# Kernel optimization log

Hardware: AMD Instinct MI355X
Metric: run time of the kernel (lower is better)

The kernel has to match this reference:

```python
import jax, jax.numpy as jnp
import numpy as np

N_NODES = 100000
N_EDGES = 100000
NNZ = 3200000
D_IN, D_HID, N_CLS = 512, 16, 7
NEG_SLOPE = 0.2


def _segment_softmax(scores, seg, num_segments, sorted_seg):
    m = jax.ops.segment_max(scores, seg, num_segments=num_segments,
                            indices_are_sorted=sorted_seg)
    ex = jnp.exp(scores - m[seg])
    s = jax.ops.segment_sum(ex, seg, num_segments=num_segments,
                            indices_are_sorted=sorted_seg)
    return ex / (s[seg] + 1e-9)


def _hypergat_layer(X, W, a1, a2, node_idx, edge_idx):
    # X: [N, din] -> h: [N, dout]
    h = X @ W
    hv = h[node_idx]                                   # [nnz, dout] gather
    # phase 1: node -> hyperedge attention (softmax within each hyperedge)
    s1 = jax.nn.leaky_relu(hv @ a1, NEG_SLOPE)         # [nnz]
    alpha = _segment_softmax(s1, edge_idx, N_EDGES, True)
    e = jax.ops.segment_sum(alpha[:, None] * hv, edge_idx,
                            num_segments=N_EDGES, indices_are_sorted=True)
    # phase 2: hyperedge -> node attention (softmax over edges incident to node)
    ev = e[edge_idx]                                   # [nnz, dout] gather
    s2 = jax.nn.leaky_relu(jnp.concatenate([hv, ev], axis=-1) @ a2, NEG_SLOPE)
    beta = _segment_softmax(s2, node_idx, N_NODES, False)
    out = jax.ops.segment_sum(beta[:, None] * ev, node_idx,
                              num_segments=N_NODES)
    return out


def setup_inputs() -> dict:
    key = jax.random.key(0)
    ks = jax.random.split(key, 8)
    H = jax.random.normal(ks[0], (N_NODES, D_IN), dtype=jnp.float32)
    node_idx = jax.random.randint(ks[1], (NNZ,), 0, N_NODES)
    edge_idx = jnp.sort(jax.random.randint(ks[2], (NNZ,), 0, N_EDGES))
    g1 = 1.0 / np.sqrt(D_IN)
    g2 = 1.0 / np.sqrt(D_HID)
    W1 = jax.random.uniform(ks[3], (D_IN, D_HID), jnp.float32, -g1, g1)
    a1_1 = jax.random.uniform(ks[4], (D_HID,), jnp.float32, -g2, g2)
    a2_1 = jax.random.uniform(ks[5], (2 * D_HID,), jnp.float32, -g2, g2)
    W2 = jax.random.uniform(ks[6], (D_HID, N_CLS), jnp.float32, -g2, g2)
    k7, k8 = jax.random.split(ks[7])
    gc = 1.0 / np.sqrt(N_CLS)
    a1_2 = jax.random.uniform(k7, (N_CLS,), jnp.float32, -gc, gc)
    a2_2 = jax.random.uniform(k8, (2 * N_CLS,), jnp.float32, -gc, gc)
    return {"H": H, "W1": W1, "a1_1": a1_1, "a2_1": a2_1,
            "W2": W2, "a1_2": a1_2, "a2_2": a2_2,
            "node_idx": node_idx, "edge_idx": edge_idx}


def reference(H, W1, a1_1, a2_1, W2, a1_2, a2_2, node_idx, edge_idx):
    H1 = _hypergat_layer(H, W1, a1_1, a2_1, node_idx, edge_idx)   # [N, 16]
    X2 = jax.nn.elu(H1)                                           # dropout off (eval)
    H2 = _hypergat_layer(X2, W2, a1_2, a2_2, node_idx, edge_idx)  # [N, 7]
    logp = jax.nn.log_softmax(H2, axis=1)
    return (logp, H1, H2)
```

## Files before the change

kernel.cpp:

```cpp
#include <hip/hip_runtime.h>
#include <hip/hip_bf16.h>
#include <math.h>

#define N_NODES 100000
#define N_EDGESC 100000
#define NNZ_C   3200000
#define D_IN    512
#define D_HID   16
#define N_CLS   7
#define NBK     782

#define G_GEMM 1563
#define G_HIST 1000
#define G_EOFF 3125
#define G_BIN  1000

typedef short short8 __attribute__((ext_vector_type(8)));
typedef float f32x4  __attribute__((ext_vector_type(4)));

__device__ __forceinline__ unsigned short f2bf_rn(float x) {
  unsigned int u = __float_as_uint(x);
  u += 0x7fff + ((u >> 16) & 1);
  return (unsigned short)(u >> 16);
}
__device__ __forceinline__ float bf2f(unsigned short b) {
  return __uint_as_float(((unsigned int)b) << 16);
}

__device__ __forceinline__ void eoff_body(int b, const int* __restrict__ eidx,
                                          int* __restrict__ eoff) {
  int i0 = (b * 256 + threadIdx.x) * 4;
  if (i0 >= NNZ_C) return;
  int4 v4 = *(const int4*)(eidx + i0);
  int vv[4] = {v4.x, v4.y, v4.z, v4.w};
  int prev = (i0 == 0) ? -1 : eidx[i0 - 1];
#pragma unroll
  for (int k = 0; k < 4; ++k) {
    for (int e = prev + 1; e <= vv[k]; ++e) eoff[e] = i0 + k;
    prev = vv[k];
  }
  if (i0 + 4 == NNZ_C) {
    for (int e = prev + 1; e <= N_EDGESC; ++e) eoff[e] = NNZ_C;
  }
}

__device__ __forceinline__ void hist_body(int b, const int* __restrict__ nidx,
                                          int* __restrict__ gcnt) {
  __shared__ int lh[NBK];
  int t = threadIdx.x;
  for (int i = t; i < NBK; i += 256) lh[i] = 0;
  __syncthreads();
  int base = b * 3200, end = base + 3200;
  for (int i = base + t; i < end; i += 256) atomicAdd(&lh[nidx[i] >> 7], 1);
  __syncthreads();
  for (int i = t; i < NBK; i += 256) {
    int c = lh[i];
    if (c) atomicAdd(&gcnt[i], c);
  }
}

__device__ __forceinline__ void bin_body(int b, const int* __restrict__ nidx,
                                         const int* __restrict__ eidx,
                                         int* __restrict__ bcur, int* __restrict__ binned) {
  __shared__ int lh[NBK];
  __shared__ int gb[NBK];
  int t = threadIdx.x;
  for (int i = t; i < NBK; i += 256) lh[i] = 0;
  __syncthreads();
  int base = b * 3200, end = base + 3200;
  for (int i = base + t; i < end; i += 256) atomicAdd(&lh[nidx[i] >> 7], 1);
  __syncthreads();
  for (int i = t; i < NBK; i += 256) {
    int c = lh[i];
    gb[i] = c ? atomicAdd(&bcur[i], c) : 0;
    lh[i] = 0;
  }
  __syncthreads();
  for (int i = base + t; i < end; i += 256) {
    int v = nidx[i], e = eidx[i];
    int bk = v >> 7;
    int r = atomicAdd(&lh[bk], 1);
    binned[gb[bk] + r] = e | ((v & 127) << 20);
  }
}

__global__ void bscan_kernel(const int* __restrict__ gcnt, int* __restrict__ boff,
                             int* __restrict__ bcur) {
  __shared__ int lds[1024];
  int t = threadIdx.x;
  int v = (t < NBK) ? gcnt[t] : 0;
  lds[t] = v;
  __syncthreads();
  for (int d = 1; d < 1024; d <<= 1) {
    int u = (t >= d) ? lds[t - d] : 0;
    __syncthreads();
    lds[t] += u;
    __syncthreads();
  }
  if (t < NBK) {
    boff[t + 1] = lds[t];
    bcur[t] = lds[t] - v;
  }
  if (t == 0) boff[0] = 0;
}

__global__ void csr_kernel(const int* __restrict__ binned, const int* __restrict__ boff,
                           int* __restrict__ noff, int* __restrict__ perm_e, int N) {
  __shared__ int lh[128];
  __shared__ int lsc[128];
  __shared__ int lcur[128];
  int b = blockIdx.x;
  int t = threadIdx.x;
  int s = boff[b], e = boff[b + 1];
  if (t < 128) lh[t] = 0;
  __syncthreads();
  for (int i = s + t; i < e; i += 256) {
    atomicAdd(&lh[binned[i] >> 20], 1);
  }
  __syncthreads();
  if (t < 128) lsc[t] = lh[t];
  __syncthreads();
  for (int d = 1; d < 128; d <<= 1) {
    int u = (t < 128 && t >= d) ? lsc[t - d] : 0;
    __syncthreads();
    if (t < 128) lsc[t] += u;
    __syncthreads();
  }
  if (t < 128) {
    int excl = lsc[t] - lh[t];
    lcur[t] = excl;
    int n = b * 128 + t;
    if (n <= N) noff[n] = s + excl;
  }
  __syncthreads();
  for (int i = s + t; i < e; i += 256) {
    int p = binned[i];
    int r = atomicAdd(&lcur[p >> 20], 1);
    perm_e[s + r] = p & 0xFFFFF;
  }
}

__device__ __forceinline__ void gemm1_body(int b,
    const float* __restrict__ X, const float* __restrict__ W,
    const float* __restrict__ a1, const float* __restrict__ a2,
    float* __restrict__ Hout, float2* __restrict__ phv) {
  int wid = b * 4 + (threadIdx.x >> 6);
  if (wid >= 6250) return;
  int lane = threadIdx.x & 63;
  int col  = lane & 15;
  int quad = lane >> 4;

  short8 wh[16], wl[16];
#pragma unroll
  for (int c = 0; c < 16; ++c) {
#pragma unroll
    for (int j = 0; j < 8; ++j) {
      float w = W[(c * 32 + quad * 8 + j) * 16 + col];
      unsigned short h = f2bf_rn(w);
      wh[c][j] = (short)h;
      wl[c][j] = (short)f2bf_rn(w - bf2f(h));
    }
  }

  int rowbase = wid * 16;
  const float4* Xr = (const float4*)(X + (size_t)(rowbase + col) * D_IN) + quad * 2;

  f32x4 acc_hh = {0.f, 0.f, 0.f, 0.f};
  f32x4 acc_hl = {0.f, 0.f, 0.f, 0.f};
  f32x4 acc_lh = {0.f, 0.f, 0.f, 0.f};

  float4 A0 = Xr[0], A1 = Xr[1];
  float4 B0 = Xr[8], B1 = Xr[9];
#pragma unroll
  for (int c = 0; c < 16; ++c) {
    float4 C0 = B0, C1 = B1;
    if (c < 14) { C0 = Xr[(c + 2) * 8]; C1 = Xr[(c + 2) * 8 + 1]; }
    float xs[8] = {A0.x, A0.y, A0.z, A0.w, A1.x, A1.y, A1.z, A1.w};
    short8 ah, al;
#pragma unroll
    for (int j = 0; j < 8; ++j) {
      unsigned short h = f2bf_rn(xs[j]);
      ah[j] = (short)h;
      al[j] = (short)f2bf_rn(xs[j] - bf2f(h));
    }
    acc_hh = __builtin_amdgcn_mfma_f32_16x16x32_bf16(ah, wh[c], acc_hh, 0, 0, 0);
    acc_hl = __builtin_amdgcn_mfma_f32_16x16x32_bf16(ah, wl[c], acc_hl, 0, 0, 0);
    acc_lh = __builtin_amdgcn_mfma_f32_16x16x32_bf16(al, wh[c], acc_lh, 0, 0, 0);
    A0 = B0; A1 = B1; B0 = C0; B1 = C1;
  }

  float a1c = a1[col], a2c = a2[col];
#pragma unroll
  for (int r = 0; r < 4; ++r) {
    float v = acc_hh[r] + acc_hl[r] + acc_lh[r];
    int row = rowbase + quad * 4 + r;
    Hout[(size_t)row * 16 + col] = v;
    float p1 = v * a1c, p2 = v * a2c;
#pragma unroll
    for (int d = 1; d < 16; d <<= 1) { p1 += __shfl_xor(p1, d); p2 += __shfl_xor(p2, d); }
    if (col == 0) phv[row] = make_float2(p1, p2);
  }
}

__global__ __launch_bounds__(256) void k1_kernel(
    const float* __restrict__ X, const float* __restrict__ W1,
    const float* __restrict__ a1_1, const float* __restrict__ a2_1,
    float* __restrict__ Hout, float2* __restrict__ phv,
    const int* __restrict__ eidx, int* __restrict__ eoff,
    const int* __restrict__ nidx, int* __restrict__ gcnt) {
  int b = blockIdx.x;
  if (b < G_GEMM) {
    gemm1_body(b, X, W1, a1_1, a2_1, Hout, phv);
  } else if (b < G_GEMM + G_HIST) {
    hist_body(b - G_GEMM, nidx, gcnt);
  } else {
    eoff_body(b - G_GEMM - G_HIST, eidx, eoff);
  }
}

template <int D, int GROUP>
__device__ __forceinline__ void edge_body(
    const float* __restrict__ h, const float2* __restrict__ phv,
    const float* __restrict__ a2, const int* __restrict__ eoff,
    const int* __restrict__ nidx, float* __restrict__ eout,
    float* __restrict__ pe, int E, int wave, int lane) {
  constexpr int NG = 64 / GROUP;
  if (wave >= E) return;
  int o0 = eoff[wave], o1 = eoff[wave + 1];
  int g = lane / GROUP, t = lane % GROUP;
  if (o0 == o1) {
    if (g == 0) {
      if (t < D) eout[(size_t)wave * D + t] = 0.f;
      if (t == 0) pe[wave] = 0.f;
    }
    return;
  }
  float m = -1e30f, l = 0.f, acc = 0.f;
  for (int base = o0; base < o1; base += 64) {
    int nrem = o1 - base; if (nrem > 64) nrem = 64;
    int li = base + lane;
    int idx_l = nidx[li < o1 ? li : o1 - 1];
    for (int jb = 0; jb < nrem; jb += 2 * NG) {
      int j = jb + g;
      bool oka = j < nrem;
      bool okb = j + NG < nrem;
      int va = __shfl(idx_l, j);
      int vb = __shfl(idx_l, j + NG);
      float pa_ = phv[va].x;
      float pb_ = phv[vb].x;
      float ha = (t < D) ? h[(size_t)va * D + t] : 0.f;
      float hb = (t < D) ? h[(size_t)vb * D + t] : 0.f;
      float sa = oka ? (pa_ > 0.f ? pa_ : 0.2f * pa_) : -1e30f;
      float sb = okb ? (pb_ > 0.f ? pb_ : 0.2f * pb_) : -1e30f;
      float mn = fmaxf(m, fmaxf(sa, sb));
      float eo = __expf(m - mn);
      float exa = oka ? __expf(sa - mn) : 0.f;
      float exb = okb ? __expf(sb - mn) : 0.f;
      l = l * eo + exa + exb;
      acc = acc * eo + exa * ha + exb * hb;
      m = mn;
    }
  }
#pragma unroll
  for (int d = GROUP; d < 64; d <<= 1) {
    float mo = __shfl_xor(m, d), lo = __shfl_xor(l, d), ao = __shfl_xor(acc, d);
    float mn = fmaxf(m, mo);
    float e0 = __expf(m - mn), e1x = __expf(mo - mn);
    l = l * e0 + lo * e1x;
    acc = acc * e0 + ao * e1x;
    m = mn;
  }
  float val = acc / (l + 1e-9f);
  float pav = (t < D) ? val * a2[D + t] : 0.f;
#pragma unroll
  for (int d = 1; d < GROUP; d <<= 1) pav += __shfl_xor(pav, d);
  if (g == 0) {
    if (t < D) eout[(size_t)wave * D + t] = val;
    if (t == 0) pe[wave] = pav;
  }
}

template <int D, int GROUP>
__global__ __launch_bounds__(256) void edge_kernel(
    const float* __restrict__ h, const float2* __restrict__ phv,
    const float* __restrict__ a2, const int* __restrict__ eoff,
    const int* __restrict__ nidx, float* __restrict__ eout,
    float* __restrict__ pe, int E) {
  int wave = (blockIdx.x * blockDim.x + threadIdx.x) >> 6;
  edge_body<D, GROUP>(h, phv, a2, eoff, nidx, eout, pe, E, wave, threadIdx.x & 63);
}

__global__ __launch_bounds__(256) void k3_kernel(
    const int* __restrict__ nidx, const int* __restrict__ eidx,
    int* __restrict__ bcur, int* __restrict__ binned,
    const float* __restrict__ h1g, const float2* __restrict__ phv,
    const float* __restrict__ a2_1, const int* __restrict__ eoff,
    float* __restrict__ e1, float* __restrict__ pe) {
  int b = blockIdx.x;
  if (b < G_BIN) {
    bin_body(b, nidx, eidx, bcur, binned);
  } else {
    int wave = (b - G_BIN) * 4 + (threadIdx.x >> 6);
    edge_body<D_HID, 16>(h1g, phv, a2_1, eoff, nidx, e1, pe, N_EDGESC,
                         wave, threadIdx.x & 63);
  }
}

__global__ __launch_bounds__(256) void node1_kernel(
    float2* phv, const float* __restrict__ e1,
    const float* __restrict__ pe, const int* __restrict__ noff,
    const int* __restrict__ perm_e, float* __restrict__ H1out,
    float* __restrict__ h2g, const float* __restrict__ W2,
    const float* __restrict__ a1_2, const float* __restrict__ a2_2) {
  int wave = (blockIdx.x * blockDim.x + threadIdx.x) >> 6;
  int lane = threadIdx.x & 63;
  if (wave >= N_NODES) return;
  int o0 = noff[wave], o1 = noff[wave + 1];
  int g = lane >> 4, t = lane & 15;
  float ph = phv[wave].y;
  float m = -1e30f, l = 0.f, acc = 0.f;
  for (int base = o0; base < o1; base += 64) {
    int nrem = o1 - base; if (nrem > 64) nrem = 64;
    int li = base + lane;
    int idx_l = perm_e[li < o1 ? li : o1 - 1];
    for (int jb = 0; jb < nrem; jb += 8) {
      int j = jb + g;
      bool oka = j < nrem;
      bool okb = j + 4 < nrem;
      int ea = __shfl(idx_l, j);
      int eb = __shfl(idx_l, j + 4);
      float pa_ = ph + pe[ea];
      float pb_ = ph + pe[eb];
      float va = e1[(size_t)ea * 16 + t];
      float vb = e1[(size_t)eb * 16 + t];
      float sa = oka ? (pa_ > 0.f ? pa_ : 0.2f * pa_) : -1e30f;
      float sb = okb ? (pb_ > 0.f ? pb_ : 0.2f * pb_) : -1e30f;
      float mn = fmaxf(m, fmaxf(sa, sb));
      float eo = __expf(m - mn);
      float exa = oka ? __expf(sa - mn) : 0.f;
      float exb = okb ? __expf(sb - mn) : 0.f;
      l = l * eo + exa + exb;
      acc = acc * eo + exa * va + exb * vb;
      m = mn;
    }
  }
#pragma unroll
  for (int d = 16; d < 64; d <<= 1) {
    float mo = __shfl_xor(m, d), lo = __shfl_xor(l, d), ao = __shfl_xor(acc, d);
    float mn = fmaxf(m, mo);
    float ea = __expf(m - mn), eb = __expf(mo - mn);
    l = l * ea + lo * eb;
    acc = acc * ea + ao * eb;
    m = mn;
  }
  float val = acc / (l + 1e-9f);
  if (g == 0) H1out[(size_t)wave * 16 + t] = val;
  float x = val > 0.f ? val : expm1f(val);
  float p1 = 0.f, p2 = 0.f, myh2 = 0.f;
#pragma unroll
  for (int j = 0; j < N_CLS; ++j) {
    float term = x * W2[t * N_CLS + j];
#pragma unroll
    for (int d = 1; d < 16; d <<= 1) term += __shfl_xor(term, d);
    p1 += term * a1_2[j];
    p2 += term * a2_2[j];
    if (t == j) myh2 = term;
  }
  if (g == 0) {
    if (t < N_CLS) h2g[(size_t)wave * N_CLS + t] = myh2;
    if (t == 0) phv[wave] = make_float2(p1, p2);
  }
}

__global__ __launch_bounds__(256) void node2_kernel(
    const float2* __restrict__ phv, const float* __restrict__ e2,
    const float* __restrict__ pe, const int* __restrict__ noff,
    const int* __restrict__ perm_e, float* __restrict__ H2out,
    float* __restrict__ logp) {
  int wave = (blockIdx.x * blockDim.x + threadIdx.x) >> 6;
  int lane = threadIdx.x & 63;
  if (wave >= N_NODES) return;
  int o0 = noff[wave], o1 = noff[wave + 1];
  int g = lane >> 3, t = lane & 7;
  float ph = phv[wave].y;
  float m = -1e30f, l = 0.f, acc = 0.f;
  for (int base = o0; base < o1; base += 64) {
    int nrem = o1 - base; if (nrem > 64) nrem = 64;
    int li = base + lane;
    int idx_l = perm_e[li < o1 ? li : o1 - 1];
    for (int jb = 0; jb < nrem; jb += 16) {
      int j = jb + g;
      bool oka = j < nrem;
      bool okb = j + 8 < nrem;
      int ea = __shfl(idx_l, j);
      int eb = __shfl(idx_l, j + 8);
      float pa_ = ph + pe[ea];
      float pb_ = ph + pe[eb];
      float va = (t < N_CLS) ? e2[(size_t)ea * N_CLS + t] : 0.f;
      float vb = (t < N_CLS) ? e2[(size_t)eb * N_CLS + t] : 0.f;
      float sa = oka ? (pa_ > 0.f ? pa_ : 0.2f * pa_) : -1e30f;
      float sb = okb ? (pb_ > 0.f ? pb_ : 0.2f * pb_) : -1e30f;
      float mn = fmaxf(m, fmaxf(sa, sb));
      float eo = __expf(m - mn);
      float exa = oka ? __expf(sa - mn) : 0.f;
      float exb = okb ? __expf(sb - mn) : 0.f;
      l = l * eo + exa + exb;
      acc = acc * eo + exa * va + exb * vb;
      m = mn;
    }
  }
#pragma unroll
  for (int d = 8; d < 64; d <<= 1) {
    float mo = __shfl_xor(m, d), lo = __shfl_xor(l, d), ao = __shfl_xor(acc, d);
    float mn = fmaxf(m, mo);
    float ea = __expf(m - mn), eb = __expf(mo - mn);
    l = l * ea + lo * eb;
    acc = acc * ea + ao * eb;
    m = mn;
  }
  float val = acc / (l + 1e-9f);
  if (g == 0 && t < N_CLS) H2out[(size_t)wave * N_CLS + t] = val;
  float xm = (t < N_CLS) ? val : -1e30f;
#pragma unroll
  for (int d = 1; d < 8; d <<= 1) xm = fmaxf(xm, __shfl_xor(xm, d));
  float se = (t < N_CLS) ? __expf(val - xm) : 0.f;
#pragma unroll
  for (int d = 1; d < 8; d <<= 1) se += __shfl_xor(se, d);
  float lg = logf(se);
  if (g == 0 && t < N_CLS) logp[(size_t)wave * N_CLS + t] = val - xm - lg;
}

extern "C" void kernel_launch(void* const* d_in, const int* in_sizes, int n_in,
                              void* d_out, int out_size, void* d_ws, size_t ws_size,
                              hipStream_t stream) {
  const float* H    = (const float*)d_in[0];
  const float* W1   = (const float*)d_in[1];
  const float* a1_1 = (const float*)d_in[2];
  const float* a2_1 = (const float*)d_in[3];
  const float* W2   = (const float*)d_in[4];
  const float* a1_2 = (const float*)d_in[5];
  const float* a2_2 = (const float*)d_in[6];
  const int* nidx   = (const int*)d_in[7];
  const int* eidx   = (const int*)d_in[8];

  float* outp = (float*)d_out;
  float* logp = outp;
  float* H1   = outp + (size_t)N_NODES * N_CLS;
  float* H2   = H1 + (size_t)N_NODES * D_HID;

  char* ws = (char*)d_ws;
  float* h1g  = (float*)(ws + 0);
  float* e1   = (float*)(ws + 6400000);
  float* h2g  = (float*)(ws + 12800000);
  float* e2   = (float*)(ws + 15600000);
  int* eoff   = (int*)(ws + 18400000);
  int* noff   = (int*)(ws + 18800128);
  float* pe   = (float*)(ws + 19200256);
  int* perm_e = (int*)(ws + 19600384);
  float2* phv = (float2*)(ws + 32400384);
  int* gcnt   = (int*)(ws + 33200384);
  int* boff   = (int*)(ws + 33203584);
  int* bcur   = (int*)(ws + 33206784);
  int* binned = (int*)(ws + 33210368);

  const int TB = 256;

  hipMemsetAsync(gcnt, 0, NBK * sizeof(int), stream);
  k1_kernel<<<G_GEMM + G_HIST + G_EOFF, TB, 0, stream>>>(
      H, W1, a1_1, a2_1, h1g, phv, eidx, eoff, nidx, gcnt);
  bscan_kernel<<<1, 1024, 0, stream>>>(gcnt, boff, bcur);
  k3_kernel<<<G_BIN + 25000, TB, 0, stream>>>(
      nidx, eidx, bcur, binned, h1g, phv, a2_1, eoff, e1, pe);
  csr_kernel<<<NBK, TB, 0, stream>>>(binned, boff, noff, perm_e, N_NODES);
  node1_kernel<<<25000, TB, 0, stream>>>(phv, e1, pe, noff, perm_e, H1, h2g,
                                         W2, a1_2, a2_2);
  edge_kernel<N_CLS, 8><<<25000, TB, 0, stream>>>(h2g, phv, a2_2, eoff, nidx, e2, pe, N_EDGESC);
  node2_kernel<<<25000, TB, 0, stream>>>(phv, e2, pe, noff, perm_e, H2, logp);
}
```

Before: 627.1 us.

## Pack layer-2 score scalars into padded 8-wide rows and unroll gather loops

Layer-2 node features and edge features are stored as 8-float rows with the attention projection scalar in the eighth slot, so one gather returns both value and score and a separate phv or pe lookup is avoided. Edge and node aggregation loops now process four neighbors per group per iteration instead of two, exposing more independent loads. The GEMM X prefetch is deepened from two chunks ahead to four. The costs are higher register pressure and padded buffers that use a little more memory traffic per row.

Result: no change. 622.5 us (-0.7%).

```diff
diff --git a/kernel.cpp b/kernel.cpp
--- a/kernel.cpp
+++ b/kernel.cpp
@@ -169,13 +169,14 @@
   f32x4 acc_hl = {0.f, 0.f, 0.f, 0.f};
   f32x4 acc_lh = {0.f, 0.f, 0.f, 0.f};
 
-  float4 A0 = Xr[0], A1 = Xr[1];
-  float4 B0 = Xr[8], B1 = Xr[9];
+  float4 pre[4][2];
+#pragma unroll
+  for (int q = 0; q < 4; ++q) { pre[q][0] = Xr[q * 8]; pre[q][1] = Xr[q * 8 + 1]; }
 #pragma unroll
   for (int c = 0; c < 16; ++c) {
-    float4 C0 = B0, C1 = B1;
-    if (c < 14) { C0 = Xr[(c + 2) * 8]; C1 = Xr[(c + 2) * 8 + 1]; }
-    float xs[8] = {A0.x, A0.y, A0.z, A0.w, A1.x, A1.y, A1.z, A1.w};
+    float4 u0 = pre[c & 3][0], u1 = pre[c & 3][1];
+    if (c < 12) { pre[c & 3][0] = Xr[(c + 4) * 8]; pre[c & 3][1] = Xr[(c + 4) * 8 + 1]; }
+    float xs[8] = {u0.x, u0.y, u0.z, u0.w, u1.x, u1.y, u1.z, u1.w};
     short8 ah, al;
 #pragma unroll
     for (int j = 0; j < 8; ++j) {
@@ -186,7 +187,6 @@
     acc_hh = __builtin_amdgcn_mfma_f32_16x16x32_bf16(ah, wh[c], acc_hh, 0, 0, 0);
     acc_hl = __builtin_amdgcn_mfma_f32_16x16x32_bf16(ah, wl[c], acc_hl, 0, 0, 0);
     acc_lh = __builtin_amdgcn_mfma_f32_16x16x32_bf16(al, wh[c], acc_lh, 0, 0, 0);
-    A0 = B0; A1 = B1; B0 = C0; B1 = C1;
   }
 
   float a1c = a1[col], a2c = a2[col];
@@ -218,19 +218,17 @@
   }
 }
 
-template <int D, int GROUP>
-__device__ __forceinline__ void edge_body(
+__device__ __forceinline__ void edge1_body(
     const float* __restrict__ h, const float2* __restrict__ phv,
     const float* __restrict__ a2, const int* __restrict__ eoff,
     const int* __restrict__ nidx, float* __restrict__ eout,
-    float* __restrict__ pe, int E, int wave, int lane) {
-  constexpr int NG = 64 / GROUP;
-  if (wave >= E) return;
+    float* __restrict__ pe, int wave, int lane) {
+  if (wave >= N_EDGESC) return;
   int o0 = eoff[wave], o1 = eoff[wave + 1];
-  int g = lane / GROUP, t = lane % GROUP;
+  int g = lane >> 4, t = lane & 15;
   if (o0 == o1) {
     if (g == 0) {
-      if (t < D) eout[(size_t)wave * D + t] = 0.f;
+      eout[(size_t)wave * 16 + t] = 0.f;
       if (t == 0) pe[wave] = 0.f;
     }
     return;
@@ -240,54 +238,50 @@
     int nrem = o1 - base; if (nrem > 64) nrem = 64;
     int li = base + lane;
     int idx_l = nidx[li < o1 ? li : o1 - 1];
-    for (int jb = 0; jb < nrem; jb += 2 * NG) {
+    for (int jb = 0; jb < nrem; jb += 16) {
       int j = jb + g;
-      bool oka = j < nrem;
-      bool okb = j + NG < nrem;
-      int va = __shfl(idx_l, j);
-      int vb = __shfl(idx_l, j + NG);
-      float pa_ = phv[va].x;
-      float pb_ = phv[vb].x;
-      float ha = (t < D) ? h[(size_t)va * D + t] : 0.f;
-      float hb = (t < D) ? h[(size_t)vb * D + t] : 0.f;
-      float sa = oka ? (pa_ > 0.f ? pa_ : 0.2f * pa_) : -1e30f;
-      float sb = okb ? (pb_ > 0.f ? pb_ : 0.2f * pb_) : -1e30f;
-      float mn = fmaxf(m, fmaxf(sa, sb));
+      bool ok0 = j < nrem, ok1 = j + 4 < nrem, ok2 = j + 8 < nrem, ok3 = j + 12 < nrem;
+      int v0 = __shfl(idx_l, j);
+      int v1 = __shfl(idx_l, j + 4);
+      int v2 = __shfl(idx_l, j + 8);
+      int v3 = __shfl(idx_l, j + 12);
+      float P0 = phv[v0].x, P1 = phv[v1].x, P2 = phv[v2].x, P3 = phv[v3].x;
+      float h0 = h[(size_t)v0 * 16 + t];
+      float h1 = h[(size_t)v1 * 16 + t];
+      float h2 = h[(size_t)v2 * 16 + t];
+      float h3 = h[(size_t)v3 * 16 + t];
+      float s0 = ok0 ? (P0 > 0.f ? P0 : 0.2f * P0) : -1e30f;
+      float s1 = ok1 ? (P1 > 0.f ? P1 : 0.2f * P1) : -1e30f;
+      float s2 = ok2 ? (P2 > 0.f ? P2 : 0.2f * P2) : -1e30f;
+      float s3 = ok3 ? (P3 > 0.f ? P3 : 0.2f * P3) : -1e30f;
+      float mn = fmaxf(fmaxf(m, fmaxf(s0, s1)), fmaxf(s2, s3));
       float eo = __expf(m - mn);
-      float exa = oka ? __expf(sa - mn) : 0.f;
-      float exb = okb ? __expf(sb - mn) : 0.f;
-      l = l * eo + exa + exb;
-      acc = acc * eo + exa * ha + exb * hb;
+      float e0 = ok0 ? __expf(s0 - mn) : 0.f;
+      float e1 = ok1 ? __expf(s1 - mn) : 0.f;
+      float e2 = ok2 ? __expf(s2 - mn) : 0.f;
+      float e3 = ok3 ? __expf(s3 - mn) : 0.f;
+      l = l * eo + ((e0 + e1) + (e2 + e3));
+      acc = acc * eo + ((e0 * h0 + e1 * h1) + (e2 * h2 + e3 * h3));
       m = mn;
     }
   }
 #pragma unroll
-  for (int d = GROUP; d < 64; d <<= 1) {
+  for (int d = 16; d < 64; d <<= 1) {
     float mo = __shfl_xor(m, d), lo = __shfl_xor(l, d), ao = __shfl_xor(acc, d);
     float mn = fmaxf(m, mo);
-    float e0 = __expf(m - mn), e1x = __expf(mo - mn);
-    l = l * e0 + lo * e1x;
-    acc = acc * e0 + ao * e1x;
+    float ea = __expf(m - mn), eb = __expf(mo - mn);
+    l = l * ea + lo * eb;
+    acc = acc * ea + ao * eb;
     m = mn;
   }
   float val = acc / (l + 1e-9f);
-  float pav = (t < D) ? val * a2[D + t] : 0.f;
-#pragma unroll
-  for (int d = 1; d < GROUP; d <<= 1) pav += __shfl_xor(pav, d);
+  float pav = val * a2[16 + t];
+#pragma unroll
+  for (int d = 1; d < 16; d <<= 1) pav += __shfl_xor(pav, d);
   if (g == 0) {
-    if (t < D) eout[(size_t)wave * D + t] = val;
+    eout[(size_t)wave * 16 + t] = val;
     if (t == 0) pe[wave] = pav;
   }
-}
-
-template <int D, int GROUP>
-__global__ __launch_bounds__(256) void edge_kernel(
-    const float* __restrict__ h, const float2* __restrict__ phv,
-    const float* __restrict__ a2, const int* __restrict__ eoff,
-    const int* __restrict__ nidx, float* __restrict__ eout,
-    float* __restrict__ pe, int E) {
-  int wave = (blockIdx.x * blockDim.x + threadIdx.x) >> 6;
-  edge_body<D, GROUP>(h, phv, a2, eoff, nidx, eout, pe, E, wave, threadIdx.x & 63);
 }
 
 __global__ __launch_bounds__(256) void k3_kernel(
@@ -301,17 +295,17 @@
     bin_body(b, nidx, eidx, bcur, binned);
   } else {
     int wave = (b - G_BIN) * 4 + (threadIdx.x >> 6);
-    edge_body<D_HID, 16>(h1g, phv, a2_1, eoff, nidx, e1, pe, N_EDGESC,
-                         wave, threadIdx.x & 63);
+    edge1_body(h1g, phv, a2_1, eoff, nidx, e1, pe, wave, threadIdx.x & 63);
   }
 }
 
 __global__ __launch_bounds__(256) void node1_kernel(
-    float2* phv, const float* __restrict__ e1,
+    const float2* __restrict__ phv, const float* __restrict__ e1,
     const float* __restrict__ pe, const int* __restrict__ noff,
     const int* __restrict__ perm_e, float* __restrict__ H1out,
-    float* __restrict__ h2g, const float* __restrict__ W2,
-    const float* __restrict__ a1_2, const float* __restrict__ a2_2) {
+    float* __restrict__ h2g8, const float* __restrict__ W2,
+    const float* __restrict__ a1_2, const float* __restrict__ a2_2,
+    float* __restrict__ pn2) {
   int wave = (blockIdx.x * blockDim.x + threadIdx.x) >> 6;
   int lane = threadIdx.x & 63;
   if (wave >= N_NODES) return;
@@ -323,89 +317,112 @@
     int nrem = o1 - base; if (nrem > 64) nrem = 64;
     int li = base + lane;
     int idx_l = perm_e[li < o1 ? li : o1 - 1];
-    for (int jb = 0; jb < nrem; jb += 8) {
+    for (int jb = 0; jb < nrem; jb += 16) {
       int j = jb + g;
-      bool oka = j < nrem;
-      bool okb = j + 4 < nrem;
-      int ea = __shfl(idx_l, j);
-      int eb = __shfl(idx_l, j + 4);
-      float pa_ = ph + pe[ea];
-      float pb_ = ph + pe[eb];
-      float va = e1[(size_t)ea * 16 + t];
-      float vb = e1[(size_t)eb * 16 + t];
-      float sa = oka ? (pa_ > 0.f ? pa_ : 0.2f * pa_) : -1e30f;
-      float sb = okb ? (pb_ > 0.f ? pb_ : 0.2f * pb_) : -1e30f;
-      float mn = fmaxf(m, fmaxf(sa, sb));
+      bool ok0 = j < nrem, ok1 = j + 4 < nrem, ok2 = j + 8 < nrem, ok3 = j + 12 < nrem;
+      int E0 = __shfl(idx_l, j);
+      int E1 = __shfl(idx_l, j + 4);
+      int E2 = __shfl(idx_l, j + 8);
+      int E3 = __shfl(idx_l, j + 12);
+      float P0 = ph + pe[E0], P1 = ph + pe[E1], P2 = ph + pe[E2], P3 = ph + pe[E3];
+      float h0 = e1[(size_t)E0 * 16 + t];
+      float h1 = e1[(size_t)E1 * 16 + t];
+      float h2 = e1[(size_t)E2 * 16 + t];
+      float h3 = e1[(size_t)E3 * 16 + t];
+      float s0 = ok0 ? (P0 > 0.f ? P0 : 0.2f * P0) : -1e30f;
+      float s1 = ok1 ? (P1 > 0.f ? P1 : 0.2f * P1) : -1e30f;
+      float s2 = ok2 ? (P2 > 0.f ? P2 : 0.2f * P2) : -1e30f;
+      float s3 = ok3 ? (P3 > 0.f ? P3 : 0.2f * P3) : -1e30f;
+      float mn = fmaxf(fmaxf(m, fmaxf(s0, s1)), fmaxf(s2, s3));
       float eo = __expf(m - mn);
-      float exa = oka ? __expf(sa - mn) : 0.f;
-      float exb = okb ? __expf(sb - mn) : 0.f;
-      l = l * eo + exa + exb;
-      acc = acc * eo + exa * va + exb * vb;
+      float e0 = ok0 ? __expf(s0 - mn) : 0.f;
+      float e1x = ok1 ? __expf(s1 - mn) : 0.f;
+      float e2x = ok2 ? __expf(s2 - mn) : 0.f;
+      float e3x = ok3 ? __expf(s3 - mn) : 0.f;
+      l = l * eo + ((e0 + e1x) + (e2x + e3x));
+      acc = acc * eo + ((e0 * h0 + e1x * h1) + (e2x * h2 + e3x * h3));
       m = mn;
     }
   }
 #pragma unroll
   for (int d = 16; d < 64; d <<= 1) {
     float mo = __shfl_xor(m, d), lo = __shfl_xor(l, d), ao = __shfl_xor(acc, d);
+    float ea_, eb_;
     float mn = fmaxf(m, mo);
-    float ea = __expf(m - mn), eb = __expf(mo - mn);
-    l = l * ea + lo * eb;
-    acc = acc * ea + ao * eb;
+    ea_ = __expf(m - mn); eb_ = __expf(mo - mn);
+    l = l * ea_ + lo * eb_;
+    acc = acc * ea_ + ao * eb_;
     m = mn;
   }
   float val = acc / (l + 1e-9f);
   if (g == 0) H1out[(size_t)wave * 16 + t] = val;
   float x = val > 0.f ? val : expm1f(val);
-  float p1 = 0.f, p2 = 0.f, myh2 = 0.f;
+  float p1 = 0.f, p2s = 0.f, myh2 = 0.f;
 #pragma unroll
   for (int j = 0; j < N_CLS; ++j) {
     float term = x * W2[t * N_CLS + j];
 #pragma unroll
     for (int d = 1; d < 16; d <<= 1) term += __shfl_xor(term, d);
     p1 += term * a1_2[j];
-    p2 += term * a2_2[j];
+    p2s += term * a2_2[j];
     if (t == j) myh2 = term;
   }
   if (g == 0) {
-    if (t < N_CLS) h2g[(size_t)wave * N_CLS + t] = myh2;
-    if (t == 0) phv[wave] = make_float2(p1, p2);
-  }
-}
-
-__global__ __launch_bounds__(256) void node2_kernel(
-    const float2* __restrict__ phv, const float* __restrict__ e2,
-    const float* __restrict__ pe, const int* __restrict__ noff,
-    const int* __restrict__ perm_e, float* __restrict__ H2out,
-    float* __restrict__ logp) {
+    if (t < N_CLS) h2g8[(size_t)wave * 8 + t] = myh2;
+    if (t == 7) h2g8[(size_t)wave * 8 + 7] = p1;
+    if (t == 0) pn2[wave] = p2s;
+  }
+}
+
+__global__ __launch_bounds__(256) void edge2_kernel(
+    const float* __restrict__ h2g8, const int* __restrict__ eoff,
+    const int* __restrict__ nidx, const float* __restrict__ a2_2,
+    float* __restrict__ e28) {
   int wave = (blockIdx.x * blockDim.x + threadIdx.x) >> 6;
   int lane = threadIdx.x & 63;
-  if (wave >= N_NODES) return;
-  int o0 = noff[wave], o1 = noff[wave + 1];
+  if (wave >= N_EDGESC) return;
+  int o0 = eoff[wave], o1 = eoff[wave + 1];
   int g = lane >> 3, t = lane & 7;
-  float ph = phv[wave].y;
+  if (o0 == o1) {
+    if (g == 0) e28[(size_t)wave * 8 + t] = 0.f;
+    return;
+  }
   float m = -1e30f, l = 0.f, acc = 0.f;
   for (int base = o0; base < o1; base += 64) {
     int nrem = o1 - base; if (nrem > 64) nrem = 64;
     int li = base + lane;
-    int idx_l = perm_e[li < o1 ? li : o1 - 1];
-    for (int jb = 0; jb < nrem; jb += 16) {
+    int idx_l = nidx[li < o1 ? li : o1 - 1];
+    for (int jb = 0; jb < nrem; jb += 32) {
       int j = jb + g;
-      bool oka = j < nrem;
-      bool okb = j + 8 < nrem;
-      int ea = __shfl(idx_l, j);
-      int eb = __shfl(idx_l, j + 8);
-      float pa_ = ph + pe[ea];
-      float pb_ = ph + pe[eb];
-      float va = (t < N_CLS) ? e2[(size_t)ea * N_CLS + t] : 0.f;
-      float vb = (t < N_CLS) ? e2[(size_t)eb * N_CLS + t] : 0.f;
-      float sa = oka ? (pa_ > 0.f ? pa_ : 0.2f * pa_) : -1e30f;
-      float sb = okb ? (pb_ > 0.f ? pb_ : 0.2f * pb_) : -1e30f;
-      float mn = fmaxf(m, fmaxf(sa, sb));
+      bool ok0 = j < nrem, ok1 = j + 8 < nrem, ok2 = j + 16 < nrem, ok3 = j + 24 < nrem;
+      int v0 = __shfl(idx_l, j);
+      int v1 = __shfl(idx_l, j + 8);
+      int v2 = __shfl(idx_l, j + 16);
+      int v3 = __shfl(idx_l, j + 24);
+      float f0 = h2g8[(size_t)v0 * 8 + t];
+      float f1 = h2g8[(size_t)v1 * 8 + t];
+      float f2 = h2g8[(size_t)v2 * 8 + t];
+      float f3 = h2g8[(size_t)v3 * 8 + t];
+      float P0 = __shfl(f0, lane | 7);
+      float P1 = __shfl(f1, lane | 7);
+      float P2 = __shfl(f2, lane | 7);
+      float P3 = __shfl(f3, lane | 7);
+      float h0 = (t < 7) ? f0 : 0.f;
+      float h1 = (t < 7) ? f1 : 0.f;
+      float h2v = (t < 7) ? f2 : 0.f;
+      float h3 = (t < 7) ? f3 : 0.f;
+      float s0 = ok0 ? (P0 > 0.f ? P0 : 0.2f * P0) : -1e30f;
+      float s1 = ok1 ? (P1 > 0.f ? P1 : 0.2f * P1) : -1e30f;
+      float s2 = ok2 ? (P2 > 0.f ? P2 : 0.2f * P2) : -1e30f;
+      float s3 = ok3 ? (P3 > 0.f ? P3 : 0.2f * P3) : -1e30f;
+      float mn = fmaxf(fmaxf(m, fmaxf(s0, s1)), fmaxf(s2, s3));
       float eo = __expf(m - mn);
-      float exa = oka ? __expf(sa - mn) : 0.f;
-      float exb = okb ? __expf(sb - mn) : 0.f;
-      l = l * eo + exa + exb;
-      acc = acc * eo + exa * va + exb * vb;
+      float e0 = ok0 ? __expf(s0 - mn) : 0.f;
+      float e1 = ok1 ? __expf(s1 - mn) : 0.f;
+      float e2 = ok2 ? __expf(s2 - mn) : 0.f;
+      float e3 = ok3 ? __expf(s3 - mn) : 0.f;
+      l = l * eo + ((e0 + e1) + (e2 + e3));
+      acc = acc * eo + ((e0 * h0 + e1 * h1) + (e2 * h2v + e3 * h3));
       m = mn;
     }
   }
@@ -419,15 +436,80 @@
     m = mn;
   }
   float val = acc / (l + 1e-9f);
-  if (g == 0 && t < N_CLS) H2out[(size_t)wave * N_CLS + t] = val;
-  float xm = (t < N_CLS) ? val : -1e30f;
+  float pav = (t < 7) ? val * a2_2[7 + t] : 0.f;
+#pragma unroll
+  for (int d = 1; d < 8; d <<= 1) pav += __shfl_xor(pav, d);
+  if (g == 0) e28[(size_t)wave * 8 + t] = (t < 7) ? val : pav;
+}
+
+__global__ __launch_bounds__(256) void node2_kernel(
+    const float* __restrict__ e28, const float* __restrict__ pn2,
+    const int* __restrict__ noff, const int* __restrict__ perm_e,
+    float* __restrict__ H2out, float* __restrict__ logp) {
+  int wave = (blockIdx.x * blockDim.x + threadIdx.x) >> 6;
+  int lane = threadIdx.x & 63;
+  if (wave >= N_NODES) return;
+  int o0 = noff[wave], o1 = noff[wave + 1];
+  int g = lane >> 3, t = lane & 7;
+  float ph = pn2[wave];
+  float m = -1e30f, l = 0.f, acc = 0.f;
+  for (int base = o0; base < o1; base += 64) {
+    int nrem = o1 - base; if (nrem > 64) nrem = 64;
+    int li = base + lane;
+    int idx_l = perm_e[li < o1 ? li : o1 - 1];
+    for (int jb = 0; jb < nrem; jb += 32) {
+      int j = jb + g;
+      bool ok0 = j < nrem, ok1 = j + 8 < nrem, ok2 = j + 16 < nrem, ok3 = j + 24 < nrem;
+      int E0 = __shfl(idx_l, j);
+      int E1 = __shfl(idx_l, j + 8);
+      int E2 = __shfl(idx_l, j + 16);
+      int E3 = __shfl(idx_l, j + 24);
+      float f0 = e28[(size_t)E0 * 8 + t];
+      float f1 = e28[(size_t)E1 * 8 + t];
+      float f2 = e28[(size_t)E2 * 8 + t];
+      float f3 = e28[(size_t)E3 * 8 + t];
+      float P0 = ph + __shfl(f0, lane | 7);
+      float P1 = ph + __shfl(f1, lane | 7);
+      float P2 = ph + __shfl(f2, lane | 7);
+      float P3 = ph + __shfl(f3, lane | 7);
+      float h0 = (t < 7) ? f0 : 0.f;
+      float h1 = (t < 7) ? f1 : 0.f;
+      float h2v = (t < 7) ? f2 : 0.f;
+      float h3 = (t < 7) ? f3 : 0.f;
+      float s0 = ok0 ? (P0 > 0.f ? P0 : 0.2f * P0) : -1e30f;
+      float s1 = ok1 ? (P1 > 0.f ? P1 : 0.2f * P1) : -1e30f;
+      float s2 = ok2 ? (P2 > 0.f ? P2 : 0.2f * P2) : -1e30f;
+      float s3 = ok3 ? (P3 > 0.f ? P3 : 0.2f * P3) : -1e30f;
+      float mn = fmaxf(fmaxf(m, fmaxf(s0, s1)), fmaxf(s2, s3));
+      float eo = __expf(m - mn);
+      float e0 = ok0 ? __expf(s0 - mn) : 0.f;
+      float e1 = ok1 ? __expf(s1 - mn) : 0.f;
+      float e2 = ok2 ? __expf(s2 - mn) : 0.f;
+      float e3 = ok3 ? __expf(s3 - mn) : 0.f;
+      l = l * eo + ((e0 + e1) + (e2 + e3));
+      acc = acc * eo + ((e0 * h0 + e1 * h1) + (e2 * h2v + e3 * h3));
+      m = mn;
+    }
+  }
+#pragma unroll
+  for (int d = 8; d < 64; d <<= 1) {
+    float mo = __shfl_xor(m, d), lo = __shfl_xor(l, d), ao = __shfl_xor(acc, d);
+    float mn = fmaxf(m, mo);
+    float ea = __expf(m - mn), eb = __expf(mo - mn);
+    l = l * ea + lo * eb;
+    acc = acc * ea + ao * eb;
+    m = mn;
+  }
+  float val = acc / (l + 1e-9f);
+  if (g == 0 && t < 7) H2out[(size_t)wave * 7 + t] = val;
+  float xm = (t < 7) ? val : -1e30f;
 #pragma unroll
   for (int d = 1; d < 8; d <<= 1) xm = fmaxf(xm, __shfl_xor(xm, d));
-  float se = (t < N_CLS) ? __expf(val - xm) : 0.f;
+  float se = (t < 7) ? __expf(val - xm) : 0.f;
 #pragma unroll
   for (int d = 1; d < 8; d <<= 1) se += __shfl_xor(se, d);
   float lg = logf(se);
-  if (g == 0 && t < N_CLS) logp[(size_t)wave * N_CLS + t] = val - xm - lg;
+  if (g == 0 && t < 7) logp[(size_t)wave * 7 + t] = val - xm - lg;
 }
 
 extern "C" void kernel_launch(void* const* d_in, const int* in_sizes, int n_in,
@@ -451,17 +533,18 @@
   char* ws = (char*)d_ws;
   float* h1g  = (float*)(ws + 0);
   float* e1   = (float*)(ws + 6400000);
-  float* h2g  = (float*)(ws + 12800000);
-  float* e2   = (float*)(ws + 15600000);
-  int* eoff   = (int*)(ws + 18400000);
-  int* noff   = (int*)(ws + 18800128);
-  float* pe   = (float*)(ws + 19200256);
-  int* perm_e = (int*)(ws + 19600384);
-  float2* phv = (float2*)(ws + 32400384);
-  int* gcnt   = (int*)(ws + 33200384);
-  int* boff   = (int*)(ws + 33203584);
-  int* bcur   = (int*)(ws + 33206784);
-  int* binned = (int*)(ws + 33210368);
+  float* h2g8 = (float*)(ws + 12800000);
+  float* e28  = (float*)(ws + 16000000);
+  int* eoff   = (int*)(ws + 19200000);
+  int* noff   = (int*)(ws + 19600128);
+  float* pe   = (float*)(ws + 20000256);
+  float* pn2  = (float*)(ws + 20400256);
+  float2* phv = (float2*)(ws + 20800256);
+  int* perm_e = (int*)(ws + 21600256);
+  int* gcnt   = (int*)(ws + 34400256);
+  int* boff   = (int*)(ws + 34403456);
+  int* bcur   = (int*)(ws + 34406656);
+  int* binned = (int*)(ws + 34409856);
 
   const int TB = 256;
 
@@ -472,8 +555,8 @@
   k3_kernel<<<G_BIN + 25000, TB, 0, stream>>>(
       nidx, eidx, bcur, binned, h1g, phv, a2_1, eoff, e1, pe);
   csr_kernel<<<NBK, TB, 0, stream>>>(binned, boff, noff, perm_e, N_NODES);
-  node1_kernel<<<25000, TB, 0, stream>>>(phv, e1, pe, noff, perm_e, H1, h2g,
-                                         W2, a1_2, a2_2);
-  edge_kernel<N_CLS, 8><<<25000, TB, 0, stream>>>(h2g, phv, a2_2, eoff, nidx, e2, pe, N_EDGESC);
-  node2_kernel<<<25000, TB, 0, stream>>>(phv, e2, pe, noff, perm_e, H2, logp);
-}
+  node1_kernel<<<25000, TB, 0, stream>>>(phv, e1, pe, noff, perm_e, H1, h2g8,
+                                         W2, a1_2, a2_2, pn2);
+  edge2_kernel<<<25000, TB, 0, stream>>>(h2g8, eoff, nidx, a2_2, e28);
+  node2_kernel<<<25000, TB, 0, stream>>>(e28, pn2, noff, perm_e, H2, logp);
+}
```
